# Kernel tuning notes

Measured on AMD Instinct MI355X. Metric: run time of the kernel, lower is better.

Reference implementation:

```python
import jax, jax.numpy as jnp
import numpy as np

POOLED_SIZES = [11, 8, 6, 4]
Q_POOLED = 2
NUM_HEADS = 2
EPS_ROUND = 1e-3  # module's self.eps used only in aspect-ratio rounding
LN_EPS = 1e-5     # torch nn.LayerNorm default


def _pool_mat(in_size, out_size):
    # PyTorch adaptive_avg_pool1d windows: start=floor(i*in/out), end=ceil((i+1)*in/out)
    M = np.zeros((out_size, in_size), np.float32)
    for i in range(out_size):
        s = (i * in_size) // out_size
        e = -(((-(i + 1)) * in_size) // out_size)
        M[i, s:e] = 1.0 / (e - s)
    return jnp.asarray(M)


def _bilinear_mat(in_size, out_size):
    # PyTorch F.interpolate bilinear, align_corners=False (half-pixel centers, clamped)
    scale = in_size / out_size
    M = np.zeros((out_size, in_size), np.float32)
    for i in range(out_size):
        src = (i + 0.5) * scale - 0.5
        src = min(max(src, 0.0), in_size - 1)
        i0 = int(np.floor(src))
        i1 = min(i0 + 1, in_size - 1)
        w = src - i0
        M[i, i0] += 1.0 - w
        M[i, i1] += w
    return jnp.asarray(M)


def _ln(x, g, b):
    m = jnp.mean(x, axis=-1, keepdims=True)
    v = jnp.mean((x - m) ** 2, axis=-1, keepdims=True)
    return (x - m) * jax.lax.rsqrt(v + LN_EPS) * g + b


def _out_size(p, H, W):
    if W >= H:
        return (p, round(W * p / H + EPS_ROUND))
    return (round(H * p / W + EPS_ROUND), p)


def setup_inputs() -> dict:
    key = jax.random.key(0)
    ks = jax.random.split(key, 12)
    B, C, H, W = 8, 32, 512, 512
    L = len(POOLED_SIZES)
    return {
        "x": jax.random.normal(ks[0], (B, C, H, W), jnp.float32),
        "q_w": jax.random.normal(ks[1], (C, C), jnp.float32) * 0.05,
        "q_b": jax.random.normal(ks[2], (C,), jnp.float32) * 0.01,
        "kv_w": jax.random.normal(ks[3], (C, 2 * C), jnp.float32) * 0.05,
        "kv_b": jax.random.normal(ks[4], (2 * C,), jnp.float32) * 0.01,
        "proj_w": jax.random.normal(ks[5], (C, C), jnp.float32) * 0.05,
        "proj_b": jax.random.normal(ks[6], (C,), jnp.float32) * 0.01,
        "norm_g": jnp.ones((C,), jnp.float32),
        "norm_b": jnp.zeros((C,), jnp.float32),
        "dconv_w": jax.random.normal(ks[7], (L, C, 1, 3, 3), jnp.float32) * 0.05,  # OIHW depthwise, stacked per level
        "dconv_b": jax.random.normal(ks[8], (L, C), jnp.float32) * 0.01,
        "H": 512,
        "W": 512,
    }


def reference(x, q_w, q_b, kv_w, kv_b, proj_w, proj_b, norm_g, norm_b, dconv_w, dconv_b, H, W):
    B, C = x.shape[0], x.shape[1]
    nh = NUM_HEADS
    hd = C // nh
    scale = hd ** (-0.5)

    # ---- query branch: adaptive pool to ~2x2, then linear ----
    qh, qw = _out_size(Q_POOLED, H, W)
    qp = jnp.einsum('ph,bchw,qw->bcpq', _pool_mat(H, qh), x, _pool_mat(W, qw))  # (B,C,qh,qw)
    qt = qp.reshape(B, C, -1).transpose(0, 2, 1)                               # (B,Nq,C)
    q = (qt @ q_w + q_b).reshape(B, -1, nh, hd).transpose(0, 2, 1, 3)          # (B,nh,Nq,hd)

    # ---- KV pyramid: adaptive pool + depthwise conv residual per level ----
    toks = []
    for i, p in enumerate(POOLED_SIZES):
        ph, pw = _out_size(p, H, W)
        pooled = jnp.einsum('ph,bchw,qw->bcpq', _pool_mat(H, ph), x, _pool_mat(W, pw))
        conv = jax.lax.conv_general_dilated(
            pooled, dconv_w[i], window_strides=(1, 1), padding='SAME',
            feature_group_count=C, dimension_numbers=('NCHW', 'OIHW', 'NCHW'))
        conv = conv + dconv_b[i][None, :, None, None]
        toks.append((pooled + conv).reshape(B, C, -1))
    toks = jnp.concatenate(toks, axis=2).transpose(0, 2, 1)  # (B,Nk,C), Nk=237
    toks = _ln(toks, norm_g, norm_b)

    kv = (toks @ kv_w + kv_b).reshape(B, -1, 2, nh, hd).transpose(2, 0, 3, 1, 4)
    k, v = kv[0], kv[1]                                       # (B,nh,Nk,hd)

    # ---- small-scale attention ----
    attn = jax.nn.softmax(jnp.einsum('bhqd,bhkd->bhqk', q, k) * scale, axis=-1)
    o = jnp.einsum('bhqk,bhkd->bhqd', attn, v).transpose(0, 2, 1, 3).reshape(B, -1, C)
    o = o @ proj_w + proj_b                                    # (B,Nq,C)

    # ---- bilinear upsample back to (H,W) ----
    o = o.transpose(0, 2, 1).reshape(B, C, qh, qw)
    out = jnp.einsum('hp,bcpq,wq->bchw', _bilinear_mat(qh, H), o, _bilinear_mat(qw, W))
    return out  # (B,C,H,W), same as module's to_4d output
```

## Files before the change

kernel.cpp:

```cpp
#include <hip/hip_runtime.h>
#include <math.h>

#define BB 8
#define CC 32
#define NTOK 241
#define NKV 237
#define YC 31

__global__ __launch_bounds__(512) void pool_kernel(const float* __restrict__ x,
                                                   float* __restrict__ pooled) {
  __shared__ float Ybuf[512 * YC];
  __shared__ float Prow[8][512];

  const int plane = blockIdx.x;
  const float* xp = x + (size_t)plane * (512 * 512);
  const int tid = threadIdx.x, wave = tid >> 6, lane = tid & 63;

  int cs = 0, ce = 1; float cinv = 0.f;
  if (lane < YC) {
    int p, jj;
    if (lane < 2)       { p = 2;  jj = lane; }
    else if (lane < 13) { p = 11; jj = lane - 2; }
    else if (lane < 21) { p = 8;  jj = lane - 13; }
    else if (lane < 27) { p = 6;  jj = lane - 21; }
    else                { p = 4;  jj = lane - 27; }
    cs = (jj * 512) / p;
    ce = ((jj + 1) * 512 + p - 1) / p;
    cinv = 1.0f / (float)(ce - cs);
  }

  float* prw = Prow[wave];

  float4 a  = *(const float4*)(xp + wave * 512 + 4 * lane);
  float4 bq = *(const float4*)(xp + wave * 512 + 256 + 4 * lane);

  for (int r = wave; r < 512; r += 8) {
    float4 an = make_float4(0.f, 0.f, 0.f, 0.f), bn = an;
    if (r + 8 < 512) {
      an = *(const float4*)(xp + (r + 8) * 512 + 4 * lane);
      bn = *(const float4*)(xp + (r + 8) * 512 + 256 + 4 * lane);
    }
    float pa0 = a.x, pa1 = pa0 + a.y, pa2 = pa1 + a.z, pa3 = pa2 + a.w;
    float pb0 = bq.x, pb1 = pb0 + bq.y, pb2 = pb1 + bq.z, pb3 = pb2 + bq.w;
    float sA = pa3, sB = pb3;
#pragma unroll
    for (int d = 1; d < 64; d <<= 1) {
      float tA = __shfl_up(sA, d);
      float tB = __shfl_up(sB, d);
      if (lane >= d) { sA += tA; sB += tB; }
    }
    float exA = sA - pa3;
    float totA = __shfl(sA, 63);
    float exB = sB - pb3 + totA;
    float4 PA = make_float4(exA + pa0, exA + pa1, exA + pa2, exA + pa3);
    float4 PB = make_float4(exB + pb0, exB + pb1, exB + pb2, exB + pb3);
    *(float4*)(prw + 4 * lane) = PA;
    *(float4*)(prw + 256 + 4 * lane) = PB;
    asm volatile("s_waitcnt lgkmcnt(0)" ::: "memory");
    if (lane < YC) {
      float sum = prw[ce - 1] - (cs ? prw[cs - 1] : 0.0f);
      Ybuf[r * YC + lane] = sum * cinv;
    }
    a = an; bq = bn;
  }
  __syncthreads();

  if (tid < NTOK) {
    int k = tid, p, colb, kb;
    if (k < 4)        { p = 2;  colb = 0;  kb = 0; }
    else if (k < 125) { p = 11; colb = 2;  kb = 4; }
    else if (k < 189) { p = 8;  colb = 13; kb = 125; }
    else if (k < 225) { p = 6;  colb = 21; kb = 189; }
    else              { p = 4;  colb = 27; kb = 225; }
    int idx = k - kb;
    int i = idx / p, j = idx - i * p;
    int s = (i * 512) / p, e = ((i + 1) * 512 + p - 1) / p;
    float s0 = 0.f, s1 = 0.f, s2 = 0.f, s3 = 0.f;
    int r = s;
    for (; r + 4 <= e; r += 4) {
      s0 += Ybuf[(r + 0) * YC + colb + j];
      s1 += Ybuf[(r + 1) * YC + colb + j];
      s2 += Ybuf[(r + 2) * YC + colb + j];
      s3 += Ybuf[(r + 3) * YC + colb + j];
    }
    for (; r < e; ++r) s0 += Ybuf[r * YC + colb + j];
    float sum = (s0 + s1) + (s2 + s3);
    pooled[(size_t)plane * NTOK + k] = sum / (float)(e - s);
  }
}

__global__ __launch_bounds__(512) void attn_kernel(
    const float* __restrict__ pooled,
    const float* __restrict__ q_w, const float* __restrict__ q_b,
    const float* __restrict__ kv_w, const float* __restrict__ kv_b,
    const float* __restrict__ proj_w, const float* __restrict__ proj_b,
    const float* __restrict__ norm_g, const float* __restrict__ norm_b,
    const float* __restrict__ dconv_w, const float* __restrict__ dconv_b,
    float* __restrict__ o_out) {
  __shared__ float pl[CC * NTOK];
  __shared__ float toks[NKV][33];
  __shared__ float kvls[NKV][65];
  __shared__ float kvw[CC * 64];
  __shared__ float dw[4 * CC * 9];
  __shared__ float dbias[4 * CC];
  __shared__ float qbias[CC], kvb[64], gln[CC], bln[CC];
  __shared__ float qtok[4][CC];
  __shared__ float attno[4][33];

  const int b = blockIdx.x, tid = threadIdx.x;
  const float* plg = pooled + (size_t)b * CC * NTOK;
  for (int i = tid; i < CC * NTOK; i += 512) pl[i] = plg[i];
  for (int i = tid; i < CC * 64; i += 512) kvw[i] = kv_w[i];
  for (int i = tid; i < 4 * CC * 9; i += 512) dw[i] = dconv_w[i];
  if (tid < 4 * CC) dbias[tid] = dconv_b[tid];
  if (tid < CC) { qbias[tid] = q_b[tid]; gln[tid] = norm_g[tid]; bln[tid] = norm_b[tid]; }
  if (tid >= 64 && tid < 128) kvb[tid - 64] = kv_b[tid - 64];
  __syncthreads();

  for (int item = tid; item < NKV * CC; item += 512) {
    int t = item >> 5, c = item & 31;
    int l, p, kb_, tb;
    if (t < 121)      { l = 0; p = 11; kb_ = 4;   tb = 0; }
    else if (t < 185) { l = 1; p = 8;  kb_ = 125; tb = 121; }
    else if (t < 221) { l = 2; p = 6;  kb_ = 189; tb = 185; }
    else              { l = 3; p = 4;  kb_ = 225; tb = 221; }
    int ti = t - tb;
    int i = ti / p, j = ti - i * p;
    const float* plc = pl + c * NTOK + kb_;
    const float* w9 = dw + (l * CC + c) * 9;
    float acc = dbias[l * CC + c];
#pragma unroll
    for (int dy = -1; dy <= 1; ++dy)
#pragma unroll
      for (int dx = -1; dx <= 1; ++dx) {
        int ii = i + dy, jj = j + dx;
        if (ii >= 0 && ii < p && jj >= 0 && jj < p)
          acc += w9[(dy + 1) * 3 + (dx + 1)] * plc[ii * p + jj];
      }
    toks[t][c] = plc[i * p + j] + acc;
  }
  __syncthreads();

  if (tid < NKV) {
    float xv[32]; float m = 0.f;
#pragma unroll
    for (int c = 0; c < 32; ++c) { xv[c] = toks[tid][c]; m += xv[c]; }
    m *= (1.0f / 32.0f);
    float v = 0.f;
#pragma unroll
    for (int c = 0; c < 32; ++c) { float d = xv[c] - m; v += d * d; }
    v *= (1.0f / 32.0f);
    float rs = rsqrtf(v + 1e-5f);
#pragma unroll
    for (int c = 0; c < 32; ++c) toks[tid][c] = (xv[c] - m) * rs * gln[c] + bln[c];
  } else if (tid >= 384) {
    int it = tid - 384;
    int n = it >> 5, u = it & 31;
    float acc = qbias[u];
#pragma unroll
    for (int c = 0; c < 32; ++c) acc += pl[c * NTOK + n] * q_w[c * 32 + u];
    qtok[n][u] = acc * 0.25f;
  }
  __syncthreads();

  for (int item = tid; item < NKV * 64; item += 512) {
    int t = item >> 6, u = item & 63;
    float acc = kvb[u];
#pragma unroll
    for (int c = 0; c < 32; ++c) acc += toks[t][c] * kvw[c * 64 + u];
    kvls[t][u] = acc;
  }
  __syncthreads();

  {
    int wave = tid >> 6, lane = tid & 63;
    int h = wave >> 2, qi = wave & 3;
    float qv[16];
#pragma unroll
    for (int d = 0; d < 16; ++d) qv[d] = qtok[qi][h * 16 + d];
    float sc[4];
#pragma unroll
    for (int m = 0; m < 4; ++m) {
      int t = lane + m * 64;
      float s = -1e30f;
      if (t < NKV) {
        s = 0.f;
#pragma unroll
        for (int d = 0; d < 16; ++d) s += qv[d] * kvls[t][h * 16 + d];
      }
      sc[m] = s;
    }
    float mx = fmaxf(fmaxf(sc[0], sc[1]), fmaxf(sc[2], sc[3]));
#pragma unroll
    for (int d = 1; d < 64; d <<= 1) mx = fmaxf(mx, __shfl_xor(mx, d));
    float pr[4]; float ssum = 0.f;
#pragma unroll
    for (int m = 0; m < 4; ++m) {
      int t = lane + m * 64;
      pr[m] = (t < NKV) ? expf(sc[m] - mx) : 0.0f;
      ssum += pr[m];
    }
#pragma unroll
    for (int d = 1; d < 64; d <<= 1) ssum += __shfl_xor(ssum, d);
    float acc[16];
#pragma unroll
    for (int d = 0; d < 16; ++d) acc[d] = 0.f;
#pragma unroll
    for (int m = 0; m < 4; ++m) {
      int t = lane + m * 64;
      if (t < NKV) {
        float p = pr[m];
#pragma unroll
        for (int d = 0; d < 16; ++d) acc[d] += p * kvls[t][32 + h * 16 + d];
      }
    }
#pragma unroll
    for (int d = 0; d < 16; ++d) {
#pragma unroll
      for (int s = 1; s < 64; s <<= 1) acc[d] += __shfl_xor(acc[d], s);
    }
    if (lane == 0) {
      float inv = 1.0f / ssum;
#pragma unroll
      for (int d = 0; d < 16; ++d) attno[qi][h * 16 + d] = acc[d] * inv;
    }
  }
  __syncthreads();

  if (tid < 128) {
    int n = tid >> 5, u = tid & 31;
    float acc = proj_b[u];
#pragma unroll
    for (int c = 0; c < 32; ++c) acc += attno[n][c] * proj_w[c * 32 + u];
    o_out[((size_t)b * 32 + u) * 4 + n] = acc;
  }
}

__global__ __launch_bounds__(256) void upsample_kernel(const float* __restrict__ o_in,
                                                       float* __restrict__ out) {
  const int plane = blockIdx.x >> 3;
  const int chunk = blockIdx.x & 7;
  const int tid = threadIdx.x;
  const int sub = tid >> 7, col4 = tid & 127;

  const float o00 = o_in[plane * 4 + 0];
  const float o01 = o_in[plane * 4 + 1];
  const float o10 = o_in[plane * 4 + 2];
  const float o11 = o_in[plane * 4 + 3];

  float top[4], bot[4];
#pragma unroll
  for (int k = 0; k < 4; ++k) {
    float c = (float)(4 * col4 + k) + 0.5f;
    float ww = c * (1.0f / 256.0f) - 0.5f;
    ww = fminf(fmaxf(ww, 0.0f), 1.0f);
    top[k] = o00 + ww * (o01 - o00);
    bot[k] = o10 + ww * (o11 - o10);
  }
  float* outp = out + (size_t)plane * (512 * 512);
  const int r0 = chunk * 64;
  for (int i = 0; i < 32; ++i) {
    int r = r0 + 2 * i + sub;
    float wh = ((float)r + 0.5f) * (1.0f / 256.0f) - 0.5f;
    wh = fminf(fmaxf(wh, 0.0f), 1.0f);
    float4 v;
    v.x = top[0] + wh * (bot[0] - top[0]);
    v.y = top[1] + wh * (bot[1] - top[1]);
    v.z = top[2] + wh * (bot[2] - top[2]);
    v.w = top[3] + wh * (bot[3] - top[3]);
    *(float4*)(outp + r * 512 + 4 * col4) = v;
  }
}

extern "C" void kernel_launch(void* const* d_in, const int* in_sizes, int n_in,
                              void* d_out, int out_size, void* d_ws, size_t ws_size,
                              hipStream_t stream) {
  const float* x       = (const float*)d_in[0];
  const float* q_w     = (const float*)d_in[1];
  const float* q_b     = (const float*)d_in[2];
  const float* kv_w    = (const float*)d_in[3];
  const float* kv_b    = (const float*)d_in[4];
  const float* proj_w  = (const float*)d_in[5];
  const float* proj_b  = (const float*)d_in[6];
  const float* norm_g  = (const float*)d_in[7];
  const float* norm_b  = (const float*)d_in[8];
  const float* dconv_w = (const float*)d_in[9];
  const float* dconv_b = (const float*)d_in[10];
  float* out = (float*)d_out;

  float* pooled = (float*)d_ws;
  float* o_ws   = pooled + (size_t)BB * CC * NTOK;

  pool_kernel<<<BB * CC, 512, 0, stream>>>(x, pooled);
  attn_kernel<<<BB, 512, 0, stream>>>(pooled, q_w, q_b, kv_w, kv_b, proj_w,
                                      proj_b, norm_g, norm_b, dconv_w, dconv_b,
                                      o_ws);
  upsample_kernel<<<BB * CC * 8, 256, 0, stream>>>(o_ws, out);
}
```

Before: 199.6 us.

## Pool columns per thread with streaming row accumulators instead of warp prefix scans

The pooling kernel now assigns one image column to each thread. Each thread streams down its 512 rows, triple-buffering 16-row register chunks, and keeps running window sums for every pool level, emitting row-pooled values into shared memory. This replaces the per-row wave prefix scan with its shuffles and LDS round-trips, and the final pass now reduces along columns. It adds many branchy per-element level checks and higher register pressure, and the 4-byte-per-lane global loads are coalesced across threads but narrower than the old float4 loads.

```diff
diff --git a/kernel.cpp b/kernel.cpp
--- a/kernel.cpp
+++ b/kernel.cpp
@@ -5,87 +5,93 @@
 #define CC 32
 #define NTOK 241
 #define NKV 237
-#define YC 31
+#define YROWS 31
+#define YPAD 520
+
+struct LvlState { int i, s, e; float acc; };
+
+template <int P, int KB>
+__device__ __forceinline__ void step_lvl(LvlState& st, float v, int r,
+                                         float (*Y)[YPAD], int c) {
+  st.acc += v;
+  if (r == st.e - 1) {
+    Y[KB + st.i][c] = st.acc * (1.0f / (float)(st.e - st.s));
+    st.i++;
+    int sn = (st.i * 512) / P;
+    st.e = ((st.i + 1) * 512 + P - 1) / P;
+    st.acc = (sn <= r) ? v : 0.0f;
+    st.s = sn;
+  }
+}
+
+__device__ __forceinline__ void load16(float (&buf)[16],
+                                       const float* __restrict__ xp, int r0) {
+#pragma unroll
+  for (int u = 0; u < 16; ++u) buf[u] = xp[(size_t)(r0 + u) * 512];
+}
+
+__device__ __forceinline__ void proc16(float (&buf)[16], int r0, LvlState& sq,
+                                       LvlState& s11, LvlState& s8,
+                                       LvlState& s6, LvlState& s4,
+                                       float (*Y)[YPAD], int c) {
+#pragma unroll
+  for (int u = 0; u < 16; ++u) {
+    float v = buf[u];
+    int r = r0 + u;
+    step_lvl<2, 0>(sq, v, r, Y, c);
+    step_lvl<11, 2>(s11, v, r, Y, c);
+    step_lvl<8, 13>(s8, v, r, Y, c);
+    step_lvl<6, 21>(s6, v, r, Y, c);
+    step_lvl<4, 27>(s4, v, r, Y, c);
+  }
+}
 
 __global__ __launch_bounds__(512) void pool_kernel(const float* __restrict__ x,
                                                    float* __restrict__ pooled) {
-  __shared__ float Ybuf[512 * YC];
-  __shared__ float Prow[8][512];
+  __shared__ float Ybuf[YROWS][YPAD];
 
   const int plane = blockIdx.x;
-  const float* xp = x + (size_t)plane * (512 * 512);
-  const int tid = threadIdx.x, wave = tid >> 6, lane = tid & 63;
-
-  int cs = 0, ce = 1; float cinv = 0.f;
-  if (lane < YC) {
-    int p, jj;
-    if (lane < 2)       { p = 2;  jj = lane; }
-    else if (lane < 13) { p = 11; jj = lane - 2; }
-    else if (lane < 21) { p = 8;  jj = lane - 13; }
-    else if (lane < 27) { p = 6;  jj = lane - 21; }
-    else                { p = 4;  jj = lane - 27; }
-    cs = (jj * 512) / p;
-    ce = ((jj + 1) * 512 + p - 1) / p;
-    cinv = 1.0f / (float)(ce - cs);
-  }
-
-  float* prw = Prow[wave];
-
-  float4 a  = *(const float4*)(xp + wave * 512 + 4 * lane);
-  float4 bq = *(const float4*)(xp + wave * 512 + 256 + 4 * lane);
-
-  for (int r = wave; r < 512; r += 8) {
-    float4 an = make_float4(0.f, 0.f, 0.f, 0.f), bn = an;
-    if (r + 8 < 512) {
-      an = *(const float4*)(xp + (r + 8) * 512 + 4 * lane);
-      bn = *(const float4*)(xp + (r + 8) * 512 + 256 + 4 * lane);
-    }
-    float pa0 = a.x, pa1 = pa0 + a.y, pa2 = pa1 + a.z, pa3 = pa2 + a.w;
-    float pb0 = bq.x, pb1 = pb0 + bq.y, pb2 = pb1 + bq.z, pb3 = pb2 + bq.w;
-    float sA = pa3, sB = pb3;
-#pragma unroll
-    for (int d = 1; d < 64; d <<= 1) {
-      float tA = __shfl_up(sA, d);
-      float tB = __shfl_up(sB, d);
-      if (lane >= d) { sA += tA; sB += tB; }
-    }
-    float exA = sA - pa3;
-    float totA = __shfl(sA, 63);
-    float exB = sB - pb3 + totA;
-    float4 PA = make_float4(exA + pa0, exA + pa1, exA + pa2, exA + pa3);
-    float4 PB = make_float4(exB + pb0, exB + pb1, exB + pb2, exB + pb3);
-    *(float4*)(prw + 4 * lane) = PA;
-    *(float4*)(prw + 256 + 4 * lane) = PB;
-    asm volatile("s_waitcnt lgkmcnt(0)" ::: "memory");
-    if (lane < YC) {
-      float sum = prw[ce - 1] - (cs ? prw[cs - 1] : 0.0f);
-      Ybuf[r * YC + lane] = sum * cinv;
-    }
-    a = an; bq = bn;
-  }
-  __syncthreads();
-
-  if (tid < NTOK) {
-    int k = tid, p, colb, kb;
-    if (k < 4)        { p = 2;  colb = 0;  kb = 0; }
-    else if (k < 125) { p = 11; colb = 2;  kb = 4; }
-    else if (k < 189) { p = 8;  colb = 13; kb = 125; }
-    else if (k < 225) { p = 6;  colb = 21; kb = 189; }
-    else              { p = 4;  colb = 27; kb = 225; }
-    int idx = k - kb;
-    int i = idx / p, j = idx - i * p;
-    int s = (i * 512) / p, e = ((i + 1) * 512 + p - 1) / p;
-    float s0 = 0.f, s1 = 0.f, s2 = 0.f, s3 = 0.f;
-    int r = s;
-    for (; r + 4 <= e; r += 4) {
-      s0 += Ybuf[(r + 0) * YC + colb + j];
-      s1 += Ybuf[(r + 1) * YC + colb + j];
-      s2 += Ybuf[(r + 2) * YC + colb + j];
-      s3 += Ybuf[(r + 3) * YC + colb + j];
-    }
-    for (; r < e; ++r) s0 += Ybuf[r * YC + colb + j];
-    float sum = (s0 + s1) + (s2 + s3);
-    pooled[(size_t)plane * NTOK + k] = sum / (float)(e - s);
+  const int c = threadIdx.x;
+  const float* xp = x + (size_t)plane * (512 * 512) + c;
+
+  LvlState sq{0, 0, 256, 0.f};
+  LvlState s11{0, 0, 47, 0.f};
+  LvlState s8{0, 0, 64, 0.f};
+  LvlState s6{0, 0, 86, 0.f};
+  LvlState s4{0, 0, 128, 0.f};
+
+  float A[16], B[16], Cb[16];
+  load16(A, xp, 0);
+  load16(B, xp, 16);
+  for (int rb = 0; rb < 480; rb += 48) {
+    load16(Cb, xp, rb + 32);
+    proc16(A, rb, sq, s11, s8, s6, s4, Ybuf, c);
+    load16(A, xp, rb + 48);
+    proc16(B, rb + 16, sq, s11, s8, s6, s4, Ybuf, c);
+    load16(B, xp, rb + 64);
+    proc16(Cb, rb + 32, sq, s11, s8, s6, s4, Ybuf, c);
+  }
+  proc16(A, 480, sq, s11, s8, s6, s4, Ybuf, c);
+  proc16(B, 496, sq, s11, s8, s6, s4, Ybuf, c);
+  __syncthreads();
+
+  if (c < NTOK) {
+    int k = c, p, kbase, kb;
+    if (k < 4)        { p = 2;  kbase = 0;  kb = 0; }
+    else if (k < 125) { p = 11; kbase = 2;  kb = 4; }
+    else if (k < 189) { p = 8;  kbase = 13; kb = 125; }
+    else if (k < 225) { p = 6;  kbase = 21; kb = 189; }
+    else              { p = 4;  kbase = 27; kb = 225; }
+    int idx = k - kb, i = idx / p, j = idx - i * p;
+    int s = (j * 512) / p, e = ((j + 1) * 512 + p - 1) / p;
+    const float* row = &Ybuf[kbase + i][0];
+    float t0 = 0.f, t1 = 0.f, t2 = 0.f, t3 = 0.f;
+    int cc = s;
+    for (; cc + 4 <= e; cc += 4) {
+      t0 += row[cc]; t1 += row[cc + 1]; t2 += row[cc + 2]; t3 += row[cc + 3];
+    }
+    for (; cc < e; ++cc) t0 += row[cc];
+    pooled[(size_t)plane * NTOK + k] = ((t0 + t1) + (t2 + t3)) / (float)(e - s);
   }
 }
 
```

Result: no change. 196.4 us (-1.6%).
